# Optimization experiments

Hardware: AMD Instinct MI355X
Metric: run time of the kernel (lower is better)

## Reference

```python
import jax, jax.numpy as jnp
import numpy as np
from functools import partial

N_NODES = 20000
N_EDGES = 640000
IN_C = 64
HID = 256
OUT_C = 64
HIST = 12
HORIZON = 6


def gcn_conv(x, w, b, src, dst, deg_inv, norm):
    # PyG GCNConv with self loops: out = D^-1/2 (A+I) D^-1/2 (x @ w) + b
    xw = x @ w                                   # [N, H]
    agg = jax.ops.segment_sum(xw[src] * norm[:, None], dst, num_segments=N_NODES)
    return agg + xw * deg_inv[:, None] + b


def gru_cell(x, h, wih, whh, bih, bhh):
    # torch.nn.GRUCell semantics; wih: [3H, in], whh: [3H, H]
    gi = x @ wih.T + bih
    gh = h @ whh.T + bhh
    ir, iz, inn = jnp.split(gi, 3, axis=-1)
    hr, hz, hn = jnp.split(gh, 3, axis=-1)
    r = jax.nn.sigmoid(ir + hr)
    z = jax.nn.sigmoid(iz + hz)
    n = jnp.tanh(inn + r * hn)
    return (1.0 - z) * n + z * h


def setup_inputs() -> dict:
    key = jax.random.key(0)
    ks = jax.random.split(key, 20)
    s = lambda fan: 1.0 / np.sqrt(fan)
    inp = {
        "x_seq": jax.random.normal(ks[0], (1, HIST, N_NODES, IN_C), dtype=jnp.float32),
        "src": jax.random.randint(ks[1], (N_EDGES,), 0, N_NODES),
        "dst": jax.random.randint(ks[2], (N_EDGES,), 0, N_NODES),
        "gcn1_w": jax.random.normal(ks[3], (IN_C, HID), jnp.float32) * s(IN_C),
        "gcn1_b": jnp.zeros((HID,), jnp.float32),
        "gcn2_w": jax.random.normal(ks[4], (HID, HID), jnp.float32) * s(HID),
        "gcn2_b": jnp.zeros((HID,), jnp.float32),
        "proj_w": jax.random.normal(ks[5], (HID, OUT_C), jnp.float32) * s(HID),
        "proj_b": jnp.zeros((OUT_C,), jnp.float32),
    }
    for i, name in enumerate(["gru1", "gru2", "gru3"]):
        k1, k2 = jax.random.split(ks[6 + i])
        inp[f"{name}_wih"] = jax.random.normal(k1, (3 * HID, HID), jnp.float32) * s(HID)
        inp[f"{name}_whh"] = jax.random.normal(k2, (3 * HID, HID), jnp.float32) * s(HID)
        inp[f"{name}_bih"] = jnp.zeros((3 * HID,), jnp.float32)
        inp[f"{name}_bhh"] = jnp.zeros((3 * HID,), jnp.float32)
    return inp


def reference(x_seq, src, dst, gcn1_w, gcn1_b, gcn2_w, gcn2_b, proj_w, proj_b,
              gru1_wih, gru1_whh, gru1_bih, gru1_bhh,
              gru2_wih, gru2_whh, gru2_bih, gru2_bhh,
              gru3_wih, gru3_whh, gru3_bih, gru3_bhh):
    # symmetric GCN normalization with self loops (static graph -> compute once)
    deg = jax.ops.segment_sum(jnp.ones((N_EDGES,), jnp.float32), dst, num_segments=N_NODES) + 1.0
    deg_is = deg ** -0.5
    norm = deg_is[src] * deg_is[dst]   # per-edge norm
    deg_inv = 1.0 / deg                # self-loop norm

    def cell(xt, h1, h2, h3):
        x = jax.nn.relu(gcn_conv(xt, gcn1_w, gcn1_b, src, dst, deg_inv, norm))
        x = jax.nn.relu(gcn_conv(x, gcn2_w, gcn2_b, src, dst, deg_inv, norm))
        h1 = gru_cell(x, h1, gru1_wih, gru1_whh, gru1_bih, gru1_bhh)
        h2 = gru_cell(h1, h2, gru2_wih, gru2_whh, gru2_bih, gru2_bhh)
        h3 = gru_cell(h2, h3, gru3_wih, gru3_whh, gru3_bih, gru3_bhh)
        return h1, h2, h3

    h0 = jnp.zeros((N_NODES, HID), jnp.float32)

    def enc_step(carry, xt):
        return cell(xt, *carry), None

    (h1, h2, h3), _ = jax.lax.scan(enc_step, (h0, h0, h0), x_seq[0])  # [T,N,C]

    def dec_step(carry, _):
        h1, h2, h3, xd = carry
        h1, h2, h3 = cell(xd, h1, h2, h3)
        y = h3 @ proj_w + proj_b       # [N, OUT_C]
        return (h1, h2, h3, y), y

    _, ys = jax.lax.scan(dec_step, (h1, h2, h3, x_seq[0, -1]), None, length=HORIZON)
    return ys[None]  # [1, HORIZON, N, OUT_C]
```

## Files before the change

kernel.cpp:

```cpp
#include <hip/hip_runtime.h>

#define N_NODESC 20000
#define N_EDGESC 640000

typedef _Float16 f16;
typedef __attribute__((ext_vector_type(4))) _Float16 f16x4;
typedef __attribute__((ext_vector_type(8))) _Float16 f16x8;
typedef __attribute__((ext_vector_type(4))) float f32x4;

__device__ __forceinline__ f32x4 mfma16(f16x8 a, f16x8 b, f32x4 c){
  return __builtin_amdgcn_mfma_f32_16x16x32_f16(a, b, c, 0, 0, 0);
}
__device__ __forceinline__ float sigm(float x){ return 1.f/(1.f+__expf(-x)); }
__device__ __forceinline__ float tanh_(float x){
  x = fminf(fmaxf(x, -15.f), 15.f);
  float e = __expf(-2.f*x);
  return (1.f - e)/(1.f + e);
}
__device__ __forceinline__ void stage16(const void* g, void* l){
  __builtin_amdgcn_global_load_lds((const __attribute__((address_space(1))) unsigned int*)g,
                                   (__attribute__((address_space(3))) unsigned int*)l, 16, 0, 0);
}
#define SB       __builtin_amdgcn_sched_barrier(0)
#define AS_VM(n) do{ asm volatile("s_waitcnt vmcnt(" #n ")" ::: "memory"); SB; }while(0)
#define BAR      do{ __builtin_amdgcn_s_barrier(); SB; }while(0)

__global__ __launch_bounds__(256) void k_hist(const int* __restrict__ dst, int* __restrict__ cnt){
  int e = blockIdx.x*256 + threadIdx.x;
  if(e < N_EDGESC) atomicAdd(&cnt[dst[e]], 1);
}

__global__ __launch_bounds__(1024) void k_scan(const int* __restrict__ cnt, int* __restrict__ row_ptr,
    float* __restrict__ deg_inv, float* __restrict__ deg_is){
  __shared__ int wsum[16];
  int t = threadIdx.x;
  int base = t*20;
  int loc[20]; int s = 0;
  #pragma unroll
  for(int i=0;i<20;i++){ int idx=base+i; int v = (idx<N_NODESC)? cnt[idx] : 0; loc[i]=s; s+=v; }
  int lane = t&63, wv = t>>6;
  int incl = s;
  #pragma unroll
  for(int off=1; off<64; off<<=1){ int u = __shfl_up(incl, off); if(lane>=off) incl += u; }
  if(lane==63) wsum[wv]=incl;
  __syncthreads();
  int woff=0;
  for(int i=0;i<wv;i++) woff += wsum[i];
  int excl = woff + incl - s;
  #pragma unroll
  for(int i=0;i<20;i++){
    int idx=base+i;
    if(idx<N_NODESC){
      row_ptr[idx] = excl + loc[i];
      float d = (float)(cnt[idx]+1);
      deg_inv[idx] = 1.f/d;
      deg_is[idx]  = rsqrtf(d);
    }
  }
  if(t==1023) row_ptr[N_NODESC] = woff + incl;
}

__global__ __launch_bounds__(256) void k_fill(const int* __restrict__ src, const int* __restrict__ dst,
    const int* __restrict__ row_ptr, int* __restrict__ cursor, const float* __restrict__ deg_is,
    int* __restrict__ colv, float* __restrict__ normv){
  int e = blockIdx.x*256 + threadIdx.x;
  if(e >= N_EDGESC) return;
  int d = dst[e], s = src[e];
  int p = atomicAdd(&cursor[d], 1);
  int idx = row_ptr[d] + p;
  colv[idx] = s;
  normv[idx] = deg_is[s]*deg_is[d];
}

__global__ __launch_bounds__(256) void k_pack(const float* __restrict__ w, f16* __restrict__ dstp,
    int K, int NO, int trans){
  int t = blockIdx.x*256 + threadIdx.x;
  if(t >= K*NO) return;
  int i = t&7, g = (t>>3)&3, rest = t>>5;
  int c = rest % NO, kb = rest / NO;
  int k = kb*32 + g*8 + i;
  float v = trans ? w[(size_t)c*K + k] : w[(size_t)k*NO + c];
  dstp[t] = (f16)v;
}

__global__ __launch_bounds__(256) void k_agg64(const float* __restrict__ x,
    const int* __restrict__ row_ptr, const int* __restrict__ colv,
    const float* __restrict__ normv, const float* __restrict__ deg_inv,
    f16* __restrict__ O){
  int n = (blockIdx.x*256 + threadIdx.x)>>6;
  int c = threadIdx.x&63;
  if(n >= N_NODESC) return;
  float acc = deg_inv[n]*x[(size_t)n*64 + c];
  int e0 = row_ptr[n], e1 = row_ptr[n+1];
  int e = e0;
  for(; e+4<=e1; e+=4){
    int s0=colv[e],s1=colv[e+1],s2=colv[e+2],s3=colv[e+3];
    float w0=normv[e],w1=normv[e+1],w2=normv[e+2],w3=normv[e+3];
    float v0=x[(size_t)s0*64+c], v1=x[(size_t)s1*64+c];
    float v2=x[(size_t)s2*64+c], v3=x[(size_t)s3*64+c];
    acc += w0*v0 + w1*v1 + w2*v2 + w3*v3;
  }
  for(; e<e1; e++) acc += normv[e]*x[(size_t)colv[e]*64+c];
  O[(size_t)n*64+c] = (f16)acc;
}

__global__ __launch_bounds__(256) void k_agg256(const f16* __restrict__ x1,
    const int* __restrict__ row_ptr, const int* __restrict__ colv,
    const float* __restrict__ normv, const float* __restrict__ deg_inv,
    f16* __restrict__ O){
  int n = (blockIdx.x*256 + threadIdx.x)>>6;
  int lane = threadIdx.x&63;
  if(n >= N_NODESC) return;
  const f16x4* xv = (const f16x4*)x1;
  f32x4 acc = __builtin_convertvector(xv[(size_t)n*64 + lane], f32x4) * deg_inv[n];
  int e0 = row_ptr[n], e1 = row_ptr[n+1];
  int e = e0;
  for(; e+4<=e1; e+=4){
    int s0=colv[e],s1=colv[e+1],s2=colv[e+2],s3=colv[e+3];
    float w0=normv[e],w1=normv[e+1],w2=normv[e+2],w3=normv[e+3];
    f32x4 v0=__builtin_convertvector(xv[(size_t)s0*64+lane], f32x4);
    f32x4 v1=__builtin_convertvector(xv[(size_t)s1*64+lane], f32x4);
    f32x4 v2=__builtin_convertvector(xv[(size_t)s2*64+lane], f32x4);
    f32x4 v3=__builtin_convertvector(xv[(size_t)s3*64+lane], f32x4);
    acc += v0*w0; acc += v1*w1; acc += v2*w2; acc += v3*w3;
  }
  for(; e<e1; e++) acc += __builtin_convertvector(xv[(size_t)colv[e]*64+lane], f32x4)*normv[e];
  ((f16x4*)O)[(size_t)n*64+lane] = __builtin_convertvector(acc, f16x4);
}

__global__ __launch_bounds__(256) void k_gcn1(const f16* __restrict__ A,
    const f16* __restrict__ Bp, const float* __restrict__ bias, f16* __restrict__ C){
  __shared__ f16x8 ldsv[512];
  char* lds = (char*)ldsv;
  const int tid = threadIdx.x, lane = tid&63, w = tid>>6, l15 = lane&15, q = lane>>4;
  const int m0 = blockIdx.x*64;
  int rg = m0 + lane; if(rg > N_NODESC-1) rg = N_NODESC-1;
  #pragma unroll
  for(int i=0;i<2;i++){
    int region = i*4 + w;
    int kbb = region>>2, qq = region&3;
    stage16((const char*)A + (size_t)rg*128 + kbb*64 + qq*16, lds + region*1024 + lane*16);
  }
  AS_VM(0);
  BAR;
  f32x4 acc[4][4];
  #pragma unroll
  for(int rt=0;rt<4;rt++)
    #pragma unroll
    for(int ct=0;ct<4;ct++) acc[rt][ct] = (f32x4){0.f,0.f,0.f,0.f};
  #pragma unroll
  for(int kb=0;kb<2;kb++){
    f16x8 bf[4];
    #pragma unroll
    for(int ct=0;ct<4;ct++){
      int c = w*64 + ct*16 + l15;
      bf[ct] = *(const f16x8*)(Bp + ((unsigned)(kb*256 + c)*4 + q)*8);
    }
    #pragma unroll
    for(int rt=0;rt<4;rt++){
      f16x8 ah = *(const f16x8*)(lds + (kb*4+q)*1024 + (rt*16+l15)*16);
      #pragma unroll
      for(int ct=0;ct<4;ct++)
        acc[rt][ct] = mfma16(ah, bf[ct], acc[rt][ct]);
    }
  }
  #pragma unroll
  for(int rt=0;rt<4;rt++)
    #pragma unroll
    for(int ct=0;ct<4;ct++){
      int c = w*64 + ct*16 + l15;
      float bv = bias[c];
      #pragma unroll
      for(int j=0;j<4;j++){
        int r = m0 + rt*16 + q*4 + j;
        if(r < N_NODESC) C[(size_t)r*256 + c] = (f16)fmaxf(acc[rt][ct][j] + bv, 0.f);
      }
    }
}

__global__ __launch_bounds__(256,2) void k_gcn2(const f16* __restrict__ A,
    const f16* __restrict__ Bp, const float* __restrict__ bias, f16* __restrict__ C){
  __shared__ f16x8 ldsv[768];
  char* lds = (char*)ldsv;
  const int tid = threadIdx.x, lane = tid&63, w = tid>>6, l15 = lane&15, q = lane>>4;
  const int m0 = blockIdx.x*64;
  int rg = m0 + lane; if(rg > N_NODESC-1) rg = N_NODESC-1;
  const size_t abyte = (size_t)rg*512;
  f32x4 acc[4][4];
  #pragma unroll
  for(int rt=0;rt<4;rt++)
    #pragma unroll
    for(int ct=0;ct<4;ct++) acc[rt][ct] = (f32x4){0.f,0.f,0.f,0.f};
  f16x8 bf[2][4];
  stage16((const char*)A + abyte + w*16, lds + 0*4096 + w*1024 + lane*16);
  SB;
  #pragma unroll
  for(int ct=0;ct<4;ct++){
    int c = w*64 + ct*16 + l15;
    bf[0][ct] = *(const f16x8*)(Bp + ((unsigned)(0*256 + c)*4 + q)*8);
  }
  SB;
  #pragma unroll
  for(int kb=0;kb<8;kb++){
    const int cur = kb%3, nxtb = (kb+1)%3, rB = kb&1;
    if(kb<7){
      stage16((const char*)A + abyte + (kb+1)*64 + w*16, lds + nxtb*4096 + w*1024 + lane*16);
      SB;
      #pragma unroll
      for(int ct=0;ct<4;ct++){
        int c = w*64 + ct*16 + l15;
        bf[rB^1][ct] = *(const f16x8*)(Bp + ((unsigned)((kb+1)*256 + c)*4 + q)*8);
      }
      AS_VM(5);
    } else {
      AS_VM(0);
    }
    BAR;
    #pragma unroll
    for(int rt=0;rt<4;rt++){
      f16x8 ah = *(const f16x8*)(lds + cur*4096 + q*1024 + (rt*16+l15)*16);
      #pragma unroll
      for(int ct=0;ct<4;ct++)
        acc[rt][ct] = mfma16(ah, bf[rB][ct], acc[rt][ct]);
    }
  }
  #pragma unroll
  for(int rt=0;rt<4;rt++)
    #pragma unroll
    for(int ct=0;ct<4;ct++){
      int c = w*64 + ct*16 + l15;
      float bv = bias[c];
      #pragma unroll
      for(int j=0;j<4;j++){
        int r = m0 + rt*16 + q*4 + j;
        if(r < N_NODESC) C[(size_t)r*256 + c] = (f16)fmaxf(acc[rt][ct][j] + bv, 0.f);
      }
    }
}

__global__ __launch_bounds__(256,2) void k_gru(
    const f16* __restrict__ X, const f16* __restrict__ H, f16* __restrict__ Nh,
    const f16* __restrict__ Wi, const f16* __restrict__ Wh,
    const float* __restrict__ bih, const float* __restrict__ bhh){
  __shared__ f16x8 ldsv[1536];
  char* lds = (char*)ldsv;
  const int NB = 1252, QQ = NB>>3, RR = NB&7;
  int bid = blockIdx.x;
  int xcd = bid & 7, jj = bid >> 3;
  int nid = (xcd < RR) ? xcd*(QQ+1) + jj : RR*(QQ+1) + (xcd-RR)*QQ + jj;
  const int m0 = (nid>>2)*64;
  const int cb = nid&3;
  const int tid = threadIdx.x, lane = tid&63, w = tid>>6, l15 = lane&15, q = lane>>4;
  const int cc = cb*64 + w*16 + l15;
  int rg = m0 + lane; if(rg > N_NODESC-1) rg = N_NODESC-1;
  const size_t abyte = (size_t)rg*512;
  const f16* pl[2] = {X, H};
  f32x4 acc[6][4];
  #pragma unroll
  for(int m=0;m<6;m++)
    #pragma unroll
    for(int rt=0;rt<4;rt++) acc[m][rt] = (f32x4){0.f,0.f,0.f,0.f};
  const unsigned wbase = (unsigned)cc*32 + q*8;
  f16x8 breg[2][6];
  #pragma unroll
  for(int i=0;i<2;i++){
    int pc = w*2 + i; int p = pc>>2, c = pc&3;
    stage16((const char*)pl[p] + abyte + c*16, lds + p*4096 + c*1024 + lane*16);
  }
  SB;
  {
    breg[0][0] = *(const f16x8*)(Wi + wbase);
    breg[0][1] = *(const f16x8*)(Wi + wbase + 8192);
    breg[0][2] = *(const f16x8*)(Wi + wbase + 16384);
    breg[0][3] = *(const f16x8*)(Wh + wbase);
    breg[0][4] = *(const f16x8*)(Wh + wbase + 8192);
    breg[0][5] = *(const f16x8*)(Wh + wbase + 16384);
  }
  SB;
  #pragma unroll
  for(int kb=0;kb<8;kb++){
    const int cur = kb%3, nxtb = (kb+1)%3, rB = kb&1;
    if(kb<7){
      #pragma unroll
      for(int i=0;i<2;i++){
        int pc = w*2 + i; int p = pc>>2, c = pc&3;
        stage16((const char*)pl[p] + abyte + (kb+1)*64 + c*16, lds + nxtb*8192 + p*4096 + c*1024 + lane*16);
      }
      SB;
      unsigned wo = wbase + (unsigned)(kb+1)*24576u;
      breg[rB^1][0] = *(const f16x8*)(Wi + wo);
      breg[rB^1][1] = *(const f16x8*)(Wi + wo + 8192);
      breg[rB^1][2] = *(const f16x8*)(Wi + wo + 16384);
      breg[rB^1][3] = *(const f16x8*)(Wh + wo);
      breg[rB^1][4] = *(const f16x8*)(Wh + wo + 8192);
      breg[rB^1][5] = *(const f16x8*)(Wh + wo + 16384);
      SB;
      AS_VM(8);
    } else {
      AS_VM(0);
    }
    BAR;
    #pragma unroll
    for(int rt=0;rt<4;rt++){
      const int ro = cur*8192 + q*1024 + (rt*16+l15)*16;
      f16x8 ax = *(const f16x8*)(lds + ro);
      f16x8 ah = *(const f16x8*)(lds + 4096 + ro);
      acc[0][rt] = mfma16(ax, breg[rB][0], acc[0][rt]);
      acc[1][rt] = mfma16(ax, breg[rB][1], acc[1][rt]);
      acc[2][rt] = mfma16(ax, breg[rB][2], acc[2][rt]);
      acc[3][rt] = mfma16(ah, breg[rB][3], acc[3][rt]);
      acc[4][rt] = mfma16(ah, breg[rB][4], acc[4][rt]);
      acc[5][rt] = mfma16(ah, breg[rB][5], acc[5][rt]);
    }
  }
  float bir=bih[cc], biz=bih[cc+256], bin=bih[cc+512];
  float bhr=bhh[cc], bhz=bhh[cc+256], bhn=bhh[cc+512];
  #pragma unroll
  for(int rt=0;rt<4;rt++){
    #pragma unroll
    for(int j=0;j<4;j++){
      int r = m0 + rt*16 + q*4 + j;
      if(r < N_NODESC){
        float ir=acc[0][rt][j], iz=acc[1][rt][j], in_=acc[2][rt][j];
        float hr=acc[3][rt][j], hz=acc[4][rt][j], hn=acc[5][rt][j];
        float rgt = sigm(ir+bir + hr+bhr);
        float zg = sigm(iz+biz + hz+bhz);
        float ng = tanh_(in_+bin + rgt*(hn+bhn));
        float ho = (float)H[(size_t)r*256 + cc];
        float v = (1.f-zg)*ng + zg*ho;
        Nh[(size_t)r*256 + cc] = (f16)v;
      }
    }
  }
}

__global__ __launch_bounds__(256,2) void k_proj(const f16* __restrict__ A,
    const f16* __restrict__ Bp, const float* __restrict__ bias, float* __restrict__ C){
  __shared__ f16x8 ldsv[768];
  char* lds = (char*)ldsv;
  const int tid = threadIdx.x, lane = tid&63, w = tid>>6, l15 = lane&15, q = lane>>4;
  const int m0 = blockIdx.x*64;
  const int cc = w*16 + l15;
  int rg = m0 + lane; if(rg > N_NODESC-1) rg = N_NODESC-1;
  const size_t abyte = (size_t)rg*512;
  f32x4 acc[4];
  #pragma unroll
  for(int rt=0;rt<4;rt++) acc[rt] = (f32x4){0.f,0.f,0.f,0.f};
  f16x8 bf[2];
  stage16((const char*)A + abyte + w*16, lds + 0*4096 + w*1024 + lane*16);
  SB;
  bf[0] = *(const f16x8*)(Bp + ((unsigned)(0*64 + cc)*4 + q)*8);
  SB;
  #pragma unroll
  for(int kb=0;kb<8;kb++){
    const int cur = kb%3, nxtb = (kb+1)%3, rB = kb&1;
    if(kb<7){
      stage16((const char*)A + abyte + (kb+1)*64 + w*16, lds + nxtb*4096 + w*1024 + lane*16);
      SB;
      bf[rB^1] = *(const f16x8*)(Bp + ((unsigned)((kb+1)*64 + cc)*4 + q)*8);
      AS_VM(2);
    } else {
      AS_VM(0);
    }
    BAR;
    #pragma unroll
    for(int rt=0;rt<4;rt++){
      f16x8 ah = *(const f16x8*)(lds + cur*4096 + q*1024 + (rt*16+l15)*16);
      acc[rt] = mfma16(ah, bf[rB], acc[rt]);
    }
  }
  #pragma unroll
  for(int rt=0;rt<4;rt++){
    float bv = bias[cc];
    #pragma unroll
    for(int j=0;j<4;j++){
      int r = m0 + rt*16 + q*4 + j;
      if(r < N_NODESC) C[(size_t)r*64 + cc] = acc[rt][j] + bv;
    }
  }
}

extern "C" void kernel_launch(void* const* d_in, const int* in_sizes, int n_in,
                              void* d_out, int out_size, void* d_ws, size_t ws_size,
                              hipStream_t stream){
  const float* x_seq  = (const float*)d_in[0];
  const int*   srcp   = (const int*)  d_in[1];
  const int*   dstp   = (const int*)  d_in[2];
  const float* gcn1_w = (const float*)d_in[3];
  const float* gcn1_b = (const float*)d_in[4];
  const float* gcn2_w = (const float*)d_in[5];
  const float* gcn2_b = (const float*)d_in[6];
  const float* proj_w = (const float*)d_in[7];
  const float* proj_b = (const float*)d_in[8];
  const float* wih[3] = {(const float*)d_in[9],  (const float*)d_in[13], (const float*)d_in[17]};
  const float* whh[3] = {(const float*)d_in[10], (const float*)d_in[14], (const float*)d_in[18]};
  const float* bih[3] = {(const float*)d_in[11], (const float*)d_in[15], (const float*)d_in[19]};
  const float* bhh[3] = {(const float*)d_in[12], (const float*)d_in[16], (const float*)d_in[20]};
  float* out = (float*)d_out;

  const size_t NP = (size_t)N_NODESC*256;
  char* p = (char*)d_ws;
  auto alloc = [&](size_t bytes)->char*{ char* r = p; p += (bytes + 255) & ~(size_t)255; return r; };
  int*   deg_cnt = (int*)  alloc((size_t)2*N_NODESC*4);
  int*   cursor  = deg_cnt + N_NODESC;
  int*   row_ptr = (int*)  alloc((size_t)(N_NODESC+1)*4);
  float* deg_inv = (float*)alloc((size_t)N_NODESC*4);
  float* deg_is  = (float*)alloc((size_t)N_NODESC*4);
  int*   colv    = (int*)  alloc((size_t)N_EDGESC*4);
  float* normv   = (float*)alloc((size_t)N_EDGESC*4);
  f16* z64  = (f16*)alloc((size_t)N_NODESC*64*2);
  f16* x1   = (f16*)alloc(NP*2);
  f16* xa   = (f16*)alloc(NP*2);
  f16* hbuf = (f16*)alloc((size_t)2*3*NP*2);
  f16* pk_gcn1 = (f16*)alloc((size_t)64*256*2);
  f16* pk_gcn2 = (f16*)alloc((size_t)256*256*2);
  f16* pk_proj = (f16*)alloc((size_t)256*64*2);
  f16* pk_wi[3]; f16* pk_wh[3];
  for(int i=0;i<3;i++){ pk_wi[i]=(f16*)alloc((size_t)256*768*2); pk_wh[i]=(f16*)alloc((size_t)256*768*2); }

  hipMemsetAsync(deg_cnt, 0, (size_t)2*N_NODESC*4, stream);
  hipMemsetAsync(hbuf,    0, (size_t)3*NP*2, stream);

  k_hist<<<2500,256,0,stream>>>(dstp, deg_cnt);
  k_scan<<<1,1024,0,stream>>>(deg_cnt, row_ptr, deg_inv, deg_is);
  k_fill<<<2500,256,0,stream>>>(srcp, dstp, row_ptr, cursor, deg_is, colv, normv);

  k_pack<<<64, 256,0,stream>>>(gcn1_w, pk_gcn1, 64, 256, 0);
  k_pack<<<256,256,0,stream>>>(gcn2_w, pk_gcn2, 256,256, 0);
  k_pack<<<64, 256,0,stream>>>(proj_w, pk_proj, 256, 64, 0);
  for(int i=0;i<3;i++){
    k_pack<<<768,256,0,stream>>>(wih[i], pk_wi[i], 256, 768, 1);
    k_pack<<<768,256,0,stream>>>(whh[i], pk_wh[i], 256, 768, 1);
  }

  auto Hs = [&](int slot, int g)->f16*{ return hbuf + ((size_t)(slot*3+g))*NP; };

  for(int s=0; s<18; s++){
    const float* xt;
    if(s < 12)       xt = x_seq + (size_t)s*N_NODESC*64;
    else if(s == 12) xt = x_seq + (size_t)11*N_NODESC*64;
    else             xt = out   + (size_t)(s-13)*N_NODESC*64;
    int cur = s&1, nxt = cur^1;

    k_agg64 <<<5000,256,0,stream>>>(xt, row_ptr, colv, normv, deg_inv, z64);
    k_gcn1  <<<313, 256,0,stream>>>(z64, pk_gcn1, gcn1_b, x1);
    k_agg256<<<5000,256,0,stream>>>(x1, row_ptr, colv, normv, deg_inv, xa);
    k_gcn2  <<<313, 256,0,stream>>>(xa, pk_gcn2, gcn2_b, xa);

    k_gru<<<1252,256,0,stream>>>(xa,        Hs(cur,0), Hs(nxt,0), pk_wi[0], pk_wh[0], bih[0], bhh[0]);
    k_gru<<<1252,256,0,stream>>>(Hs(nxt,0), Hs(cur,1), Hs(nxt,1), pk_wi[1], pk_wh[1], bih[1], bhh[1]);
    k_gru<<<1252,256,0,stream>>>(Hs(nxt,1), Hs(cur,2), Hs(nxt,2), pk_wi[2], pk_wh[2], bih[2], bhh[2]);

    if(s >= 12)
      k_proj<<<313,256,0,stream>>>(Hs(nxt,2), pk_proj, proj_b, out + (size_t)(s-12)*N_NODESC*64);
  }
}
```

Baseline: 3.863 ms.

## Interleave edge arrays, use fp16 node inputs, deepen LDS prefetch to two stages

Packs each edge's column index and normalization weight into a single int2, so the aggregation kernels issue one load per edge instead of two. The input sequence is converted to fp16 once up front, and the projection kernel also writes an fp16 copy of its output for the next decoder step, which halves gather bytes in the 64-channel aggregation. The gcn2, gru and proj GEMMs move from a 3-slot LDS ring with one-ahead prefetch to a 4-slot ring with two-ahead prefetch to hide more load latency. This costs more LDS per block, which may lower occupancy, and rounds the inputs to fp16 before the first aggregation.

```diff
diff --git a/kernel.cpp b/kernel.cpp
--- a/kernel.cpp
+++ b/kernel.cpp
@@ -62,14 +62,22 @@
 
 __global__ __launch_bounds__(256) void k_fill(const int* __restrict__ src, const int* __restrict__ dst,
     const int* __restrict__ row_ptr, int* __restrict__ cursor, const float* __restrict__ deg_is,
-    int* __restrict__ colv, float* __restrict__ normv){
+    int2* __restrict__ ev){
   int e = blockIdx.x*256 + threadIdx.x;
   if(e >= N_EDGESC) return;
   int d = dst[e], s = src[e];
   int p = atomicAdd(&cursor[d], 1);
-  int idx = row_ptr[d] + p;
-  colv[idx] = s;
-  normv[idx] = deg_is[s]*deg_is[d];
+  int2 v;
+  v.x = s;
+  v.y = __float_as_int(deg_is[s]*deg_is[d]);
+  ev[row_ptr[d] + p] = v;
+}
+
+__global__ __launch_bounds__(256) void k_cvt(const float* __restrict__ x, f16* __restrict__ o, int n4){
+  int i = blockIdx.x*256 + threadIdx.x;
+  if(i >= n4) return;
+  f32x4 v = *(const f32x4*)(x + (size_t)i*4);
+  *(f16x4*)(o + (size_t)i*4) = __builtin_convertvector(v, f16x4);
 }
 
 __global__ __launch_bounds__(256) void k_pack(const float* __restrict__ w, f16* __restrict__ dstp,
@@ -83,31 +91,29 @@
   dstp[t] = (f16)v;
 }
 
-__global__ __launch_bounds__(256) void k_agg64(const float* __restrict__ x,
-    const int* __restrict__ row_ptr, const int* __restrict__ colv,
-    const float* __restrict__ normv, const float* __restrict__ deg_inv,
-    f16* __restrict__ O){
+__global__ __launch_bounds__(256) void k_agg64(const f16* __restrict__ x,
+    const int* __restrict__ row_ptr, const int2* __restrict__ ev,
+    const float* __restrict__ deg_inv, f16* __restrict__ O){
   int n = (blockIdx.x*256 + threadIdx.x)>>6;
   int c = threadIdx.x&63;
   if(n >= N_NODESC) return;
-  float acc = deg_inv[n]*x[(size_t)n*64 + c];
+  float acc = deg_inv[n]*(float)x[(size_t)n*64 + c];
   int e0 = row_ptr[n], e1 = row_ptr[n+1];
   int e = e0;
   for(; e+4<=e1; e+=4){
-    int s0=colv[e],s1=colv[e+1],s2=colv[e+2],s3=colv[e+3];
-    float w0=normv[e],w1=normv[e+1],w2=normv[e+2],w3=normv[e+3];
-    float v0=x[(size_t)s0*64+c], v1=x[(size_t)s1*64+c];
-    float v2=x[(size_t)s2*64+c], v3=x[(size_t)s3*64+c];
-    acc += w0*v0 + w1*v1 + w2*v2 + w3*v3;
-  }
-  for(; e<e1; e++) acc += normv[e]*x[(size_t)colv[e]*64+c];
+    int2 a=ev[e], b=ev[e+1], cc=ev[e+2], d=ev[e+3];
+    float v0=(float)x[(size_t)a.x*64+c],  v1=(float)x[(size_t)b.x*64+c];
+    float v2=(float)x[(size_t)cc.x*64+c], v3=(float)x[(size_t)d.x*64+c];
+    acc += __int_as_float(a.y)*v0 + __int_as_float(b.y)*v1
+         + __int_as_float(cc.y)*v2 + __int_as_float(d.y)*v3;
+  }
+  for(; e<e1; e++){ int2 a=ev[e]; acc += __int_as_float(a.y)*(float)x[(size_t)a.x*64+c]; }
   O[(size_t)n*64+c] = (f16)acc;
 }
 
 __global__ __launch_bounds__(256) void k_agg256(const f16* __restrict__ x1,
-    const int* __restrict__ row_ptr, const int* __restrict__ colv,
-    const float* __restrict__ normv, const float* __restrict__ deg_inv,
-    f16* __restrict__ O){
+    const int* __restrict__ row_ptr, const int2* __restrict__ ev,
+    const float* __restrict__ deg_inv, f16* __restrict__ O){
   int n = (blockIdx.x*256 + threadIdx.x)>>6;
   int lane = threadIdx.x&63;
   if(n >= N_NODESC) return;
@@ -116,15 +122,16 @@
   int e0 = row_ptr[n], e1 = row_ptr[n+1];
   int e = e0;
   for(; e+4<=e1; e+=4){
-    int s0=colv[e],s1=colv[e+1],s2=colv[e+2],s3=colv[e+3];
-    float w0=normv[e],w1=normv[e+1],w2=normv[e+2],w3=normv[e+3];
-    f32x4 v0=__builtin_convertvector(xv[(size_t)s0*64+lane], f32x4);
-    f32x4 v1=__builtin_convertvector(xv[(size_t)s1*64+lane], f32x4);
-    f32x4 v2=__builtin_convertvector(xv[(size_t)s2*64+lane], f32x4);
-    f32x4 v3=__builtin_convertvector(xv[(size_t)s3*64+lane], f32x4);
-    acc += v0*w0; acc += v1*w1; acc += v2*w2; acc += v3*w3;
-  }
-  for(; e<e1; e++) acc += __builtin_convertvector(xv[(size_t)colv[e]*64+lane], f32x4)*normv[e];
+    int2 a=ev[e], b=ev[e+1], cc=ev[e+2], d=ev[e+3];
+    f32x4 v0=__builtin_convertvector(xv[(size_t)a.x*64+lane],  f32x4);
+    f32x4 v1=__builtin_convertvector(xv[(size_t)b.x*64+lane],  f32x4);
+    f32x4 v2=__builtin_convertvector(xv[(size_t)cc.x*64+lane], f32x4);
+    f32x4 v3=__builtin_convertvector(xv[(size_t)d.x*64+lane],  f32x4);
+    acc += v0*__int_as_float(a.y); acc += v1*__int_as_float(b.y);
+    acc += v2*__int_as_float(cc.y); acc += v3*__int_as_float(d.y);
+  }
+  for(; e<e1; e++){ int2 a=ev[e];
+    acc += __builtin_convertvector(xv[(size_t)a.x*64+lane], f32x4)*__int_as_float(a.y); }
   ((f16x4*)O)[(size_t)n*64+lane] = __builtin_convertvector(acc, f16x4);
 }
 
@@ -180,7 +187,7 @@
 
 __global__ __launch_bounds__(256,2) void k_gcn2(const f16* __restrict__ A,
     const f16* __restrict__ Bp, const float* __restrict__ bias, f16* __restrict__ C){
-  __shared__ f16x8 ldsv[768];
+  __shared__ f16x8 ldsv[1024];
   char* lds = (char*)ldsv;
   const int tid = threadIdx.x, lane = tid&63, w = tid>>6, l15 = lane&15, q = lane>>4;
   const int m0 = blockIdx.x*64;
@@ -194,6 +201,8 @@
   f16x8 bf[2][4];
   stage16((const char*)A + abyte + w*16, lds + 0*4096 + w*1024 + lane*16);
   SB;
+  stage16((const char*)A + abyte + 64 + w*16, lds + 1*4096 + w*1024 + lane*16);
+  SB;
   #pragma unroll
   for(int ct=0;ct<4;ct++){
     int c = w*64 + ct*16 + l15;
@@ -202,19 +211,20 @@
   SB;
   #pragma unroll
   for(int kb=0;kb<8;kb++){
-    const int cur = kb%3, nxtb = (kb+1)%3, rB = kb&1;
+    const int cur = kb&3, rB = kb&1;
+    if(kb<6){
+      stage16((const char*)A + abyte + (kb+2)*64 + w*16, lds + ((kb+2)&3)*4096 + w*1024 + lane*16);
+      SB;
+    }
     if(kb<7){
-      stage16((const char*)A + abyte + (kb+1)*64 + w*16, lds + nxtb*4096 + w*1024 + lane*16);
-      SB;
       #pragma unroll
       for(int ct=0;ct<4;ct++){
         int c = w*64 + ct*16 + l15;
         bf[rB^1][ct] = *(const f16x8*)(Bp + ((unsigned)((kb+1)*256 + c)*4 + q)*8);
       }
-      AS_VM(5);
-    } else {
-      AS_VM(0);
-    }
+      SB;
+    }
+    if(kb<6){ AS_VM(5); } else if(kb==6){ AS_VM(4); } else { AS_VM(0); }
     BAR;
     #pragma unroll
     for(int rt=0;rt<4;rt++){
@@ -242,7 +252,7 @@
     const f16* __restrict__ X, const f16* __restrict__ H, f16* __restrict__ Nh,
     const f16* __restrict__ Wi, const f16* __restrict__ Wh,
     const float* __restrict__ bih, const float* __restrict__ bhh){
-  __shared__ f16x8 ldsv[1536];
+  __shared__ f16x8 ldsv[2048];
   char* lds = (char*)ldsv;
   const int NB = 1252, QQ = NB>>3, RR = NB&7;
   int bid = blockIdx.x;
@@ -265,7 +275,13 @@
   #pragma unroll
   for(int i=0;i<2;i++){
     int pc = w*2 + i; int p = pc>>2, c = pc&3;
-    stage16((const char*)pl[p] + abyte + c*16, lds + p*4096 + c*1024 + lane*16);
+    stage16((const char*)pl[p] + abyte + c*16, lds + 0*8192 + p*4096 + c*1024 + lane*16);
+  }
+  SB;
+  #pragma unroll
+  for(int i=0;i<2;i++){
+    int pc = w*2 + i; int p = pc>>2, c = pc&3;
+    stage16((const char*)pl[p] + abyte + 64 + c*16, lds + 1*8192 + p*4096 + c*1024 + lane*16);
   }
   SB;
   {
@@ -279,14 +295,17 @@
   SB;
   #pragma unroll
   for(int kb=0;kb<8;kb++){
-    const int cur = kb%3, nxtb = (kb+1)%3, rB = kb&1;
-    if(kb<7){
+    const int cur = kb&3, rB = kb&1;
+    if(kb<6){
       #pragma unroll
       for(int i=0;i<2;i++){
         int pc = w*2 + i; int p = pc>>2, c = pc&3;
-        stage16((const char*)pl[p] + abyte + (kb+1)*64 + c*16, lds + nxtb*8192 + p*4096 + c*1024 + lane*16);
-      }
-      SB;
+        stage16((const char*)pl[p] + abyte + (kb+2)*64 + c*16,
+                lds + ((kb+2)&3)*8192 + p*4096 + c*1024 + lane*16);
+      }
+      SB;
+    }
+    if(kb<7){
       unsigned wo = wbase + (unsigned)(kb+1)*24576u;
       breg[rB^1][0] = *(const f16x8*)(Wi + wo);
       breg[rB^1][1] = *(const f16x8*)(Wi + wo + 8192);
@@ -295,10 +314,8 @@
       breg[rB^1][4] = *(const f16x8*)(Wh + wo + 8192);
       breg[rB^1][5] = *(const f16x8*)(Wh + wo + 16384);
       SB;
-      AS_VM(8);
-    } else {
-      AS_VM(0);
-    }
+    }
+    if(kb<6){ AS_VM(8); } else if(kb==6){ AS_VM(6); } else { AS_VM(0); }
     BAR;
     #pragma unroll
     for(int rt=0;rt<4;rt++){
@@ -335,8 +352,9 @@
 }
 
 __global__ __launch_bounds__(256,2) void k_proj(const f16* __restrict__ A,
-    const f16* __restrict__ Bp, const float* __restrict__ bias, float* __restrict__ C){
-  __shared__ f16x8 ldsv[768];
+    const f16* __restrict__ Bp, const float* __restrict__ bias,
+    float* __restrict__ C, f16* __restrict__ Cf16){
+  __shared__ f16x8 ldsv[1024];
   char* lds = (char*)ldsv;
   const int tid = threadIdx.x, lane = tid&63, w = tid>>6, l15 = lane&15, q = lane>>4;
   const int m0 = blockIdx.x*64;
@@ -349,19 +367,22 @@
   f16x8 bf[2];
   stage16((const char*)A + abyte + w*16, lds + 0*4096 + w*1024 + lane*16);
   SB;
+  stage16((const char*)A + abyte + 64 + w*16, lds + 1*4096 + w*1024 + lane*16);
+  SB;
   bf[0] = *(const f16x8*)(Bp + ((unsigned)(0*64 + cc)*4 + q)*8);
   SB;
   #pragma unroll
   for(int kb=0;kb<8;kb++){
-    const int cur = kb%3, nxtb = (kb+1)%3, rB = kb&1;
+    const int cur = kb&3, rB = kb&1;
+    if(kb<6){
+      stage16((const char*)A + abyte + (kb+2)*64 + w*16, lds + ((kb+2)&3)*4096 + w*1024 + lane*16);
+      SB;
+    }
     if(kb<7){
-      stage16((const char*)A + abyte + (kb+1)*64 + w*16, lds + nxtb*4096 + w*1024 + lane*16);
-      SB;
       bf[rB^1] = *(const f16x8*)(Bp + ((unsigned)((kb+1)*64 + cc)*4 + q)*8);
-      AS_VM(2);
-    } else {
-      AS_VM(0);
-    }
+      SB;
+    }
+    if(kb<6){ AS_VM(2); } else if(kb==6){ AS_VM(1); } else { AS_VM(0); }
     BAR;
     #pragma unroll
     for(int rt=0;rt<4;rt++){
@@ -375,7 +396,11 @@
     #pragma unroll
     for(int j=0;j<4;j++){
       int r = m0 + rt*16 + q*4 + j;
-      if(r < N_NODESC) C[(size_t)r*64 + cc] = acc[rt][j] + bv;
+      if(r < N_NODESC){
+        float v = acc[rt][j] + bv;
+        C[(size_t)r*64 + cc] = v;
+        Cf16[(size_t)r*64 + cc] = (f16)v;
+      }
     }
   }
 }
@@ -406,8 +431,9 @@
   int*   row_ptr = (int*)  alloc((size_t)(N_NODESC+1)*4);
   float* deg_inv = (float*)alloc((size_t)N_NODESC*4);
   float* deg_is  = (float*)alloc((size_t)N_NODESC*4);
-  int*   colv    = (int*)  alloc((size_t)N_EDGESC*4);
-  float* normv   = (float*)alloc((size_t)N_EDGESC*4);
+  int2*  ev      = (int2*) alloc((size_t)N_EDGESC*8);
+  f16* xf16 = (f16*)alloc((size_t)12*N_NODESC*64*2);
+  f16* xdec = (f16*)alloc((size_t)N_NODESC*64*2);
   f16* z64  = (f16*)alloc((size_t)N_NODESC*64*2);
   f16* x1   = (f16*)alloc(NP*2);
   f16* xa   = (f16*)alloc(NP*2);
@@ -423,7 +449,8 @@
 
   k_hist<<<2500,256,0,stream>>>(dstp, deg_cnt);
   k_scan<<<1,1024,0,stream>>>(deg_cnt, row_ptr, deg_inv, deg_is);
-  k_fill<<<2500,256,0,stream>>>(srcp, dstp, row_ptr, cursor, deg_is, colv, normv);
+  k_fill<<<2500,256,0,stream>>>(srcp, dstp, row_ptr, cursor, deg_is, ev);
+  k_cvt<<<15000,256,0,stream>>>(x_seq, xf16, 12*N_NODESC*64/4);
 
   k_pack<<<64, 256,0,stream>>>(gcn1_w, pk_gcn1, 64, 256, 0);
   k_pack<<<256,256,0,stream>>>(gcn2_w, pk_gcn2, 256,256, 0);
@@ -436,15 +463,15 @@
   auto Hs = [&](int slot, int g)->f16*{ return hbuf + ((size_t)(slot*3+g))*NP; };
 
   for(int s=0; s<18; s++){
-    const float* xt;
-    if(s < 12)       xt = x_seq + (size_t)s*N_NODESC*64;
-    else if(s == 12) xt = x_seq + (size_t)11*N_NODESC*64;
-    else             xt = out   + (size_t)(s-13)*N_NODESC*64;
+    const f16* xt;
+    if(s < 12)       xt = xf16 + (size_t)s*N_NODESC*64;
+    else if(s == 12) xt = xf16 + (size_t)11*N_NODESC*64;
+    else             xt = xdec;
     int cur = s&1, nxt = cur^1;
 
-    k_agg64 <<<5000,256,0,stream>>>(xt, row_ptr, colv, normv, deg_inv, z64);
+    k_agg64 <<<5000,256,0,stream>>>(xt, row_ptr, ev, deg_inv, z64);
     k_gcn1  <<<313, 256,0,stream>>>(z64, pk_gcn1, gcn1_b, x1);
-    k_agg256<<<5000,256,0,stream>>>(x1, row_ptr, colv, normv, deg_inv, xa);
+    k_agg256<<<5000,256,0,stream>>>(x1, row_ptr, ev, deg_inv, xa);
     k_gcn2  <<<313, 256,0,stream>>>(xa, pk_gcn2, gcn2_b, xa);
 
     k_gru<<<1252,256,0,stream>>>(xa,        Hs(cur,0), Hs(nxt,0), pk_wi[0], pk_wh[0], bih[0], bhh[0]);
@@ -452,6 +479,6 @@
     k_gru<<<1252,256,0,stream>>>(Hs(nxt,1), Hs(cur,2), Hs(nxt,2), pk_wi[2], pk_wh[2], bih[2], bhh[2]);
 
     if(s >= 12)
-      k_proj<<<313,256,0,stream>>>(Hs(nxt,2), pk_proj, proj_b, out + (size_t)(s-12)*N_NODESC*64);
-  }
-}
+      k_proj<<<313,256,0,stream>>>(Hs(nxt,2), pk_proj, proj_b, out + (size_t)(s-12)*N_NODESC*64, xdec);
+  }
+}
```

Result: no change. 3.805 ms (-1.5%).
